# Kernel tuning notes

Measured on AMD Instinct MI355X. Metric: run time of the kernel, lower is better.

Reference implementation:

```python
import jax, jax.numpy as jnp
import numpy as np

N_NODES = 100000
N_EDGES = 1600000
IN_CH = 128
OUT_CH = 64
HEADS = 2
EDGE_DIM = 32


def _fake_quant(w):
    # 8-bit signed symmetric fake quantization (brevitas-style) with STE
    scale = jnp.max(jnp.abs(w)) / 127.0 + 1e-12
    q = jnp.clip(jnp.round(w / scale), -128.0, 127.0) * scale
    return w + jax.lax.stop_gradient(q - w)


def setup_inputs() -> dict:
    key = jax.random.key(0)
    ks = jax.random.split(key, 9)
    x = jax.random.normal(ks[0], (N_NODES, IN_CH), dtype=jnp.float32)
    edge_index = jax.random.randint(ks[1], (2, N_EDGES), 0, N_NODES, dtype=jnp.int64)
    edge_attr = jax.random.normal(ks[2], (N_EDGES, EDGE_DIM), dtype=jnp.float32)
    w_lin = jax.random.normal(ks[3], (HEADS * OUT_CH, IN_CH), dtype=jnp.float32) * (1.0 / np.sqrt(IN_CH))
    w_edge = jax.random.normal(ks[4], (HEADS * OUT_CH, EDGE_DIM), dtype=jnp.float32) * (1.0 / np.sqrt(EDGE_DIM))
    att_src = jax.random.normal(ks[5], (1, HEADS, OUT_CH), dtype=jnp.float32) * 0.1
    att_dst = jax.random.normal(ks[6], (1, HEADS, OUT_CH), dtype=jnp.float32) * 0.1
    att_edge = jax.random.normal(ks[7], (1, HEADS, OUT_CH), dtype=jnp.float32) * 0.1
    bias = jnp.zeros((OUT_CH,), dtype=jnp.float32)
    return {"x": x, "edge_index": edge_index, "edge_attr": edge_attr,
            "w_lin": w_lin, "w_edge": w_edge, "att_src": att_src,
            "att_dst": att_dst, "att_edge": att_edge, "bias": bias}


def reference(x, edge_index, edge_attr, w_lin, w_edge, att_src, att_dst, att_edge, bias):
    N = x.shape[0]
    src, dst = edge_index[0], edge_index[1]
    # quantized linear projection (int8 fake-quant weights)
    xp = (x @ _fake_quant(w_lin).T).reshape(N, HEADS, OUT_CH)  # [N,H,C]
    # per-node attention logits
    a_src = jnp.sum(xp * att_src, axis=-1)  # [N,H]
    a_dst = jnp.sum(xp * att_dst, axis=-1)  # [N,H]
    # edge feature projection + edge attention logits
    ep = (edge_attr @ w_edge.T).reshape(-1, HEADS, OUT_CH)      # [E,H,C]
    a_edge = jnp.sum(ep * att_edge, axis=-1)                    # [E,H]
    alpha = a_src[src] + a_dst[dst] + a_edge                    # [E,H]
    alpha = jax.nn.leaky_relu(alpha, negative_slope=0.2)
    # segment softmax over edges grouped by destination node
    amax = jax.ops.segment_max(alpha, dst, num_segments=N)      # [N,H]
    ex = jnp.exp(alpha - amax[dst])
    denom = jax.ops.segment_sum(ex, dst, num_segments=N)        # [N,H]
    coef = ex / (denom[dst] + 1e-16)                            # [E,H]
    # gather source messages, weight, scatter-add to destinations
    msg = xp[src] * coef[:, :, None]                            # [E,H,C]
    out = jax.ops.segment_sum(msg, dst, num_segments=N)         # [N,H,C]
    out = jnp.mean(out, axis=1) + bias                          # concat=False -> head mean
    # QuantIdentity on output (8-bit activation fake-quant)
    return _fake_quant(out)
```

## Files before the change

kernel.cpp:

```cpp
#include <hip/hip_runtime.h>
#include <math.h>

#define N_NODES 100000
#define N_EDGES 1600000
#define IN_CH 128
#define OUT_CH 64
#define HC 128
#define EDGE_DIM 32

__global__ __launch_bounds__(256) void k_prep(const float* __restrict__ w_lin,
                                              const float* __restrict__ w_edge,
                                              const float* __restrict__ att_edge,
                                              float* __restrict__ qw,
                                              float* __restrict__ ve) {
    __shared__ float red[256];
    __shared__ float sscale;
    int t = threadIdx.x;
    float m = 0.f;
    for (int i = t; i < HC * IN_CH; i += 256) m = fmaxf(m, fabsf(w_lin[i]));
    red[t] = m;
    __syncthreads();
    for (int off = 128; off > 0; off >>= 1) {
        if (t < off) red[t] = fmaxf(red[t], red[t + off]);
        __syncthreads();
    }
    if (t == 0) sscale = red[0] / 127.0f + 1e-12f;
    __syncthreads();
    float scale = sscale;
    for (int i = t; i < HC * IN_CH; i += 256) {
        float q = rintf(w_lin[i] / scale);
        q = fminf(127.f, fmaxf(-128.f, q));
        qw[i] = q * scale;
    }
    if (t < 64) {
        int h = t >> 5, k = t & 31;
        float s = 0.f;
        for (int c = 0; c < OUT_CH; ++c)
            s += att_edge[h * OUT_CH + c] * w_edge[(h * OUT_CH + c) * EDGE_DIM + k];
        ve[h * EDGE_DIM + k] = s;
    }
}

__global__ __launch_bounds__(256) void k_proj(const float* __restrict__ x,
                                              const float* __restrict__ qw,
                                              float* __restrict__ xp) {
    __shared__ float xs[128 * 128];
    const int nb = blockIdx.x * 128;
    for (int i = threadIdx.x; i < 4096; i += 256) {
        int w = i << 2;
        int row = w >> 7;
        int col = w & 127;
        int gn = nb + row;
        float4 v = make_float4(0.f, 0.f, 0.f, 0.f);
        if (gn < N_NODES) v = *(const float4*)(x + (size_t)gn * IN_CH + col);
        int scol = col ^ (((row >> 3) & 3) << 2);
        *(float4*)(&xs[row * 128 + scol]) = v;
    }
    __syncthreads();
    const int cg = threadIdx.x & 15;
    const int ng = threadIdx.x >> 4;
    const int c0 = cg << 3;
    const int n0 = ng << 3;
    float acc[8][8];
#pragma unroll
    for (int i = 0; i < 8; i++)
#pragma unroll
        for (int j = 0; j < 8; j++) acc[i][j] = 0.f;

    const int swz = ((ng & 3) << 2);
    for (int k = 0; k < 128; k += 4) {
        float4 xv[8], wv[8];
#pragma unroll
        for (int i = 0; i < 8; i++)
            xv[i] = *(const float4*)(&xs[(n0 + i) * 128 + (k ^ swz)]);
#pragma unroll
        for (int j = 0; j < 8; j++)
            wv[j] = *(const float4*)(qw + (c0 + j) * IN_CH + k);
#pragma unroll
        for (int i = 0; i < 8; i++)
#pragma unroll
            for (int j = 0; j < 8; j++)
                acc[i][j] += xv[i].x * wv[j].x + xv[i].y * wv[j].y +
                             xv[i].z * wv[j].z + xv[i].w * wv[j].w;
    }
#pragma unroll
    for (int i = 0; i < 8; i++) {
        int gn = nb + n0 + i;
        if (gn < N_NODES) {
            float4 o0 = make_float4(acc[i][0], acc[i][1], acc[i][2], acc[i][3]);
            float4 o1 = make_float4(acc[i][4], acc[i][5], acc[i][6], acc[i][7]);
            *(float4*)(xp + (size_t)gn * HC + c0) = o0;
            *(float4*)(xp + (size_t)gn * HC + c0 + 4) = o1;
        }
    }
}

__global__ __launch_bounds__(256) void k_attn_node(const float* __restrict__ xp,
                                                   const float* __restrict__ att_src,
                                                   const float* __restrict__ att_dst,
                                                   float* __restrict__ a_src,
                                                   float* __restrict__ a_dst) {
    int n = blockIdx.x * 4 + (threadIdx.x >> 6);
    int lane = threadIdx.x & 63;
    if (n >= N_NODES) return;
    float x0 = xp[(size_t)n * HC + lane];
    float x1 = xp[(size_t)n * HC + 64 + lane];
    float s0 = x0 * att_src[lane];
    float s1 = x1 * att_src[64 + lane];
    float d0 = x0 * att_dst[lane];
    float d1 = x1 * att_dst[64 + lane];
    for (int off = 32; off > 0; off >>= 1) {
        s0 += __shfl_xor(s0, off, 64);
        s1 += __shfl_xor(s1, off, 64);
        d0 += __shfl_xor(d0, off, 64);
        d1 += __shfl_xor(d1, off, 64);
    }
    if (lane == 0) {
        ((float2*)a_src)[n] = make_float2(s0, s1);
        ((float2*)a_dst)[n] = make_float2(d0, d1);
    }
}

__global__ __launch_bounds__(256) void k_edge(const int* __restrict__ ei,
                                              const float* __restrict__ ea,
                                              const float* __restrict__ ve,
                                              const float* __restrict__ a_src,
                                              const float* __restrict__ a_dst,
                                              float* __restrict__ alpha,
                                              int* __restrict__ counts) {
    __shared__ float lds[256 * 33];
    __shared__ float vel[64];
    int t = threadIdx.x;
    int base = blockIdx.x * 256;
    if (t < 64) vel[t] = ve[t];
    for (int i = t; i < 256 * EDGE_DIM; i += 256)
        lds[(i >> 5) * 33 + (i & 31)] = ea[(size_t)base * EDGE_DIM + i];
    __syncthreads();
    int e = base + t;
    int src = ei[e];
    int dst = ei[N_EDGES + e];
    float ae0 = 0.f, ae1 = 0.f;
    const float* row = &lds[t * 33];
#pragma unroll
    for (int k = 0; k < 32; k++) {
        ae0 += row[k] * vel[k];
        ae1 += row[k] * vel[32 + k];
    }
    float2 as = ((const float2*)a_src)[src];
    float2 ad = ((const float2*)a_dst)[dst];
    float al0 = as.x + ad.x + ae0;
    float al1 = as.y + ad.y + ae1;
    al0 = al0 >= 0.f ? al0 : 0.2f * al0;
    al1 = al1 >= 0.f ? al1 : 0.2f * al1;
    ((float2*)alpha)[e] = make_float2(al0, al1);
    atomicAdd(&counts[dst], 1);
}

__global__ __launch_bounds__(256) void k_bsum(const int* __restrict__ counts, int* __restrict__ bsums) {
    __shared__ int s[256];
    int i = blockIdx.x * 256 + threadIdx.x;
    int v = (i < N_NODES) ? counts[i] : 0;
    s[threadIdx.x] = v;
    __syncthreads();
    for (int off = 128; off > 0; off >>= 1) {
        if (threadIdx.x < off) s[threadIdx.x] += s[threadIdx.x + off];
        __syncthreads();
    }
    if (threadIdx.x == 0) bsums[blockIdx.x] = s[0];
}

__global__ __launch_bounds__(512) void k_bscan(const int* __restrict__ bsums, int* __restrict__ boff, int nb) {
    __shared__ int s[512];
    int t = threadIdx.x;
    int v = (t < nb) ? bsums[t] : 0;
    s[t] = v;
    __syncthreads();
    for (int off = 1; off < 512; off <<= 1) {
        int add = (t >= off) ? s[t - off] : 0;
        __syncthreads();
        s[t] += add;
        __syncthreads();
    }
    if (t < nb) boff[t] = s[t] - v;
}

__global__ __launch_bounds__(256) void k_offsets(const int* __restrict__ counts,
                                                 const int* __restrict__ boff,
                                                 int* __restrict__ offsets) {
    __shared__ int s[256];
    int t = threadIdx.x;
    int i = blockIdx.x * 256 + t;
    int v = (i < N_NODES) ? counts[i] : 0;
    s[t] = v;
    __syncthreads();
    for (int off = 1; off < 256; off <<= 1) {
        int add = (t >= off) ? s[t - off] : 0;
        __syncthreads();
        s[t] += add;
        __syncthreads();
    }
    if (i < N_NODES) offsets[i] = boff[blockIdx.x] + s[t] - v;
    if (i == 0) offsets[N_NODES] = N_EDGES;
}

__global__ __launch_bounds__(256) void k_scatter(const int* __restrict__ ei,
                                                 const float* __restrict__ alpha,
                                                 int* __restrict__ cursors,
                                                 int* __restrict__ src_sorted,
                                                 float* __restrict__ alpha_sorted) {
    int e = blockIdx.x * 256 + threadIdx.x;
    int src = ei[e];
    int dst = ei[N_EDGES + e];
    float2 a = ((const float2*)alpha)[e];
    int pos = atomicAdd(&cursors[dst], 1);
    src_sorted[pos] = src;
    ((float2*)alpha_sorted)[pos] = a;
}

__global__ __launch_bounds__(256) void k_aggregate(const int* __restrict__ offsets,
                                                   const int* __restrict__ src_sorted,
                                                   const float* __restrict__ alpha_sorted,
                                                   const float* __restrict__ xp,
                                                   const float* __restrict__ bias,
                                                   float* __restrict__ out) {
    int n = blockIdx.x * 4 + (threadIdx.x >> 6);
    if (n >= N_NODES) return;
    int lane = threadIdx.x & 63;
    int start = offsets[n], end = offsets[n + 1];
    float m0 = -INFINITY, m1 = -INFINITY;
    for (int j = start + lane; j < end; j += 64) {
        float2 a = ((const float2*)alpha_sorted)[j];
        m0 = fmaxf(m0, a.x);
        m1 = fmaxf(m1, a.y);
    }
    for (int off = 32; off > 0; off >>= 1) {
        m0 = fmaxf(m0, __shfl_xor(m0, off, 64));
        m1 = fmaxf(m1, __shfl_xor(m1, off, 64));
    }
    float accA = 0.f, accB = 0.f, d0 = 0.f, d1 = 0.f;
    int j = start;
    int s_next = 0;
    float2 a_next = make_float2(0.f, 0.f);
    if (j < end) {
        s_next = src_sorted[j];
        a_next = ((const float2*)alpha_sorted)[j];
    }
    for (; j < end; ++j) {
        int sc = s_next;
        float2 ac = a_next;
        if (j + 1 < end) {
            s_next = src_sorted[j + 1];
            a_next = ((const float2*)alpha_sorted)[j + 1];
        }
        float ex0 = expf(ac.x - m0);
        float ex1 = expf(ac.y - m1);
        d0 += ex0;
        d1 += ex1;
        const float* r = xp + (size_t)sc * HC;
        accA += ex0 * r[lane];
        accB += ex1 * r[64 + lane];
    }
    float o = 0.5f * (accA / (d0 + 1e-16f) + accB / (d1 + 1e-16f)) + bias[lane];
    out[(size_t)n * OUT_CH + lane] = o;
}

__global__ __launch_bounds__(256) void k_absmax(const float* __restrict__ v, unsigned int* __restrict__ amax) {
    float m = 0.f;
    int stride = gridDim.x * 256;
    for (int i = blockIdx.x * 256 + threadIdx.x; i < N_NODES * OUT_CH / 4; i += stride) {
        float4 x = ((const float4*)v)[i];
        m = fmaxf(m, fmaxf(fmaxf(fabsf(x.x), fabsf(x.y)), fmaxf(fabsf(x.z), fabsf(x.w))));
    }
    for (int off = 32; off > 0; off >>= 1) m = fmaxf(m, __shfl_xor(m, off, 64));
    if ((threadIdx.x & 63) == 0) atomicMax(amax, __float_as_uint(m));
}

__global__ __launch_bounds__(256) void k_quant_out(float* __restrict__ v, const unsigned int* __restrict__ amax) {
    float scale = __uint_as_float(*amax) / 127.0f + 1e-12f;
    int i = blockIdx.x * 256 + threadIdx.x;
    float4 x = ((const float4*)v)[i];
    float qx = fminf(127.f, fmaxf(-128.f, rintf(x.x / scale)));
    float qy = fminf(127.f, fmaxf(-128.f, rintf(x.y / scale)));
    float qz = fminf(127.f, fmaxf(-128.f, rintf(x.z / scale)));
    float qw_ = fminf(127.f, fmaxf(-128.f, rintf(x.w / scale)));
    ((float4*)v)[i] = make_float4(qx * scale, qy * scale, qz * scale, qw_ * scale);
}

extern "C" void kernel_launch(void* const* d_in, const int* in_sizes, int n_in,
                              void* d_out, int out_size, void* d_ws, size_t ws_size,
                              hipStream_t stream) {
    const float* x        = (const float*)d_in[0];
    const int*   ei       = (const int*)d_in[1];
    const float* ea       = (const float*)d_in[2];
    const float* w_lin    = (const float*)d_in[3];
    const float* w_edge   = (const float*)d_in[4];
    const float* att_src  = (const float*)d_in[5];
    const float* att_dst  = (const float*)d_in[6];
    const float* att_edge = (const float*)d_in[7];
    const float* bias     = (const float*)d_in[8];
    float* out = (float*)d_out;

    char* ws = (char*)d_ws;
    size_t off = 0;
    auto alloc = [&](size_t b) {
        void* p = ws + off;
        off = (off + b + 255) & ~(size_t)255;
        return p;
    };
    float* qw           = (float*)alloc((size_t)HC * IN_CH * 4);
    float* ve           = (float*)alloc(64 * 4);
    float* xp           = (float*)alloc((size_t)N_NODES * HC * 4);
    float* a_src        = (float*)alloc((size_t)N_NODES * 2 * 4);
    float* a_dst        = (float*)alloc((size_t)N_NODES * 2 * 4);
    float* alpha        = (float*)alloc((size_t)N_EDGES * 2 * 4);
    int*   counts       = (int*)alloc((size_t)N_NODES * 4);
    int*   offsets      = (int*)alloc((size_t)(N_NODES + 1) * 4);
    int*   cursors      = (int*)alloc((size_t)N_NODES * 4);
    int*   bsums        = (int*)alloc(512 * 4);
    int*   boff         = (int*)alloc(512 * 4);
    int*   src_sorted   = (int*)alloc((size_t)N_EDGES * 4);
    float* alpha_sorted = (float*)alloc((size_t)N_EDGES * 2 * 4);
    unsigned int* amax  = (unsigned int*)alloc(256);

    hipMemsetAsync(counts, 0, (size_t)N_NODES * 4, stream);
    hipMemsetAsync(amax, 0, 4, stream);

    k_prep<<<1, 256, 0, stream>>>(w_lin, w_edge, att_edge, qw, ve);
    k_proj<<<(N_NODES + 127) / 128, 256, 0, stream>>>(x, qw, xp);
    k_attn_node<<<(N_NODES + 3) / 4, 256, 0, stream>>>(xp, att_src, att_dst, a_src, a_dst);
    k_edge<<<N_EDGES / 256, 256, 0, stream>>>(ei, ea, ve, a_src, a_dst, alpha, counts);
    int nb = (N_NODES + 255) / 256;
    k_bsum<<<nb, 256, 0, stream>>>(counts, bsums);
    k_bscan<<<1, 512, 0, stream>>>(bsums, boff, nb);
    k_offsets<<<nb, 256, 0, stream>>>(counts, boff, offsets);
    hipMemcpyAsync(cursors, offsets, (size_t)N_NODES * 4, hipMemcpyDeviceToDevice, stream);
    k_scatter<<<N_EDGES / 256, 256, 0, stream>>>(ei, alpha, cursors, src_sorted, alpha_sorted);
    k_aggregate<<<(N_NODES + 3) / 4, 256, 0, stream>>>(offsets, src_sorted, alpha_sorted, xp, bias, out);
    k_absmax<<<1024, 256, 0, stream>>>(out, amax);
    k_quant_out<<<(N_NODES * OUT_CH / 4) / 256, 256, 0, stream>>>(out, amax);
}
```

Baseline: 880.8 us.

## Use bf16 MFMA split-precision projection, fuse node logits, merge alpha into scatter

The projection GEMM moves from fp32 FMA to bf16 MFMA. The int8-valued weights are stored exactly in bf16 and x is split into high and low bf16 parts to keep near-fp32 accuracy, with the scale applied afterwards. The node attention logits are computed in the GEMM epilogue, which removes a separate pass over xp. Edge alpha computation is moved into the scatter kernel, so the intermediate alpha array is no longer written and reread, and a light count kernel does the degree histogram. The aggregate kernel also switches to fast __expf, and the split-bf16 path adds a small rounding error compared with pure fp32.

```diff
diff --git a/kernel.cpp b/kernel.cpp
--- a/kernel.cpp
+++ b/kernel.cpp
@@ -8,10 +8,14 @@
 #define HC 128
 #define EDGE_DIM 32
 
+typedef __bf16 bf16x8 __attribute__((ext_vector_type(8)));
+typedef float f32x4 __attribute__((ext_vector_type(4)));
+
 __global__ __launch_bounds__(256) void k_prep(const float* __restrict__ w_lin,
                                               const float* __restrict__ w_edge,
                                               const float* __restrict__ att_edge,
-                                              float* __restrict__ qw,
+                                              __bf16* __restrict__ qwb,
+                                              float* __restrict__ qscale,
                                               float* __restrict__ ve) {
     __shared__ float red[256];
     __shared__ float sscale;
@@ -24,13 +28,13 @@
         if (t < off) red[t] = fmaxf(red[t], red[t + off]);
         __syncthreads();
     }
-    if (t == 0) sscale = red[0] / 127.0f + 1e-12f;
+    if (t == 0) { sscale = red[0] / 127.0f + 1e-12f; qscale[0] = sscale; }
     __syncthreads();
     float scale = sscale;
     for (int i = t; i < HC * IN_CH; i += 256) {
         float q = rintf(w_lin[i] / scale);
         q = fminf(127.f, fmaxf(-128.f, q));
-        qw[i] = q * scale;
+        qwb[i] = (__bf16)q;
     }
     if (t < 64) {
         int h = t >> 5, k = t & 31;
@@ -42,118 +46,124 @@
 }
 
 __global__ __launch_bounds__(256) void k_proj(const float* __restrict__ x,
-                                              const float* __restrict__ qw,
-                                              float* __restrict__ xp) {
-    __shared__ float xs[128 * 128];
-    const int nb = blockIdx.x * 128;
-    for (int i = threadIdx.x; i < 4096; i += 256) {
-        int w = i << 2;
-        int row = w >> 7;
-        int col = w & 127;
-        int gn = nb + row;
-        float4 v = make_float4(0.f, 0.f, 0.f, 0.f);
-        if (gn < N_NODES) v = *(const float4*)(x + (size_t)gn * IN_CH + col);
-        int scol = col ^ (((row >> 3) & 3) << 2);
-        *(float4*)(&xs[row * 128 + scol]) = v;
-    }
-    __syncthreads();
-    const int cg = threadIdx.x & 15;
-    const int ng = threadIdx.x >> 4;
-    const int c0 = cg << 3;
-    const int n0 = ng << 3;
-    float acc[8][8];
-#pragma unroll
-    for (int i = 0; i < 8; i++)
-#pragma unroll
-        for (int j = 0; j < 8; j++) acc[i][j] = 0.f;
-
-    const int swz = ((ng & 3) << 2);
-    for (int k = 0; k < 128; k += 4) {
-        float4 xv[8], wv[8];
-#pragma unroll
-        for (int i = 0; i < 8; i++)
-            xv[i] = *(const float4*)(&xs[(n0 + i) * 128 + (k ^ swz)]);
-#pragma unroll
-        for (int j = 0; j < 8; j++)
-            wv[j] = *(const float4*)(qw + (c0 + j) * IN_CH + k);
-#pragma unroll
-        for (int i = 0; i < 8; i++)
-#pragma unroll
-            for (int j = 0; j < 8; j++)
-                acc[i][j] += xv[i].x * wv[j].x + xv[i].y * wv[j].y +
-                             xv[i].z * wv[j].z + xv[i].w * wv[j].w;
-    }
-#pragma unroll
-    for (int i = 0; i < 8; i++) {
-        int gn = nb + n0 + i;
-        if (gn < N_NODES) {
-            float4 o0 = make_float4(acc[i][0], acc[i][1], acc[i][2], acc[i][3]);
-            float4 o1 = make_float4(acc[i][4], acc[i][5], acc[i][6], acc[i][7]);
-            *(float4*)(xp + (size_t)gn * HC + c0) = o0;
-            *(float4*)(xp + (size_t)gn * HC + c0 + 4) = o1;
-        }
-    }
-}
-
-__global__ __launch_bounds__(256) void k_attn_node(const float* __restrict__ xp,
-                                                   const float* __restrict__ att_src,
-                                                   const float* __restrict__ att_dst,
-                                                   float* __restrict__ a_src,
-                                                   float* __restrict__ a_dst) {
-    int n = blockIdx.x * 4 + (threadIdx.x >> 6);
-    int lane = threadIdx.x & 63;
-    if (n >= N_NODES) return;
-    float x0 = xp[(size_t)n * HC + lane];
-    float x1 = xp[(size_t)n * HC + 64 + lane];
-    float s0 = x0 * att_src[lane];
-    float s1 = x1 * att_src[64 + lane];
-    float d0 = x0 * att_dst[lane];
-    float d1 = x1 * att_dst[64 + lane];
-    for (int off = 32; off > 0; off >>= 1) {
-        s0 += __shfl_xor(s0, off, 64);
-        s1 += __shfl_xor(s1, off, 64);
-        d0 += __shfl_xor(d0, off, 64);
-        d1 += __shfl_xor(d1, off, 64);
-    }
-    if (lane == 0) {
-        ((float2*)a_src)[n] = make_float2(s0, s1);
-        ((float2*)a_dst)[n] = make_float2(d0, d1);
-    }
-}
-
-__global__ __launch_bounds__(256) void k_edge(const int* __restrict__ ei,
-                                              const float* __restrict__ ea,
-                                              const float* __restrict__ ve,
-                                              const float* __restrict__ a_src,
-                                              const float* __restrict__ a_dst,
-                                              float* __restrict__ alpha,
-                                              int* __restrict__ counts) {
-    __shared__ float lds[256 * 33];
-    __shared__ float vel[64];
-    int t = threadIdx.x;
-    int base = blockIdx.x * 256;
-    if (t < 64) vel[t] = ve[t];
-    for (int i = t; i < 256 * EDGE_DIM; i += 256)
-        lds[(i >> 5) * 33 + (i & 31)] = ea[(size_t)base * EDGE_DIM + i];
-    __syncthreads();
-    int e = base + t;
-    int src = ei[e];
-    int dst = ei[N_EDGES + e];
-    float ae0 = 0.f, ae1 = 0.f;
-    const float* row = &lds[t * 33];
-#pragma unroll
-    for (int k = 0; k < 32; k++) {
-        ae0 += row[k] * vel[k];
-        ae1 += row[k] * vel[32 + k];
-    }
-    float2 as = ((const float2*)a_src)[src];
-    float2 ad = ((const float2*)a_dst)[dst];
-    float al0 = as.x + ad.x + ae0;
-    float al1 = as.y + ad.y + ae1;
-    al0 = al0 >= 0.f ? al0 : 0.2f * al0;
-    al1 = al1 >= 0.f ? al1 : 0.2f * al1;
-    ((float2*)alpha)[e] = make_float2(al0, al1);
-    atomicAdd(&counts[dst], 1);
+                                              const __bf16* __restrict__ qwb,
+                                              const float* __restrict__ qscale,
+                                              const float* __restrict__ att_src,
+                                              const float* __restrict__ att_dst,
+                                              float* __restrict__ xp,
+                                              float* __restrict__ a_src,
+                                              float* __restrict__ a_dst) {
+    const int wave = threadIdx.x >> 6;
+    const int lane = threadIdx.x & 63;
+    const int cl = lane & 15;
+    const int kg = lane >> 4;
+    const int nb = blockIdx.x * 128 + wave * 32;
+
+    f32x4 acc[2][8];
+#pragma unroll
+    for (int mt = 0; mt < 2; ++mt)
+#pragma unroll
+        for (int nt = 0; nt < 8; ++nt)
+            acc[mt][nt] = (f32x4){0.f, 0.f, 0.f, 0.f};
+
+    const int kb0 = kg * 8;
+#pragma unroll
+    for (int kc = 0; kc < 4; ++kc) {
+        const int kb = kc * 32 + kb0;
+        bf16x8 ah[2], al[2];
+#pragma unroll
+        for (int mt = 0; mt < 2; ++mt) {
+            int row = nb + mt * 16 + cl;
+            float v[8];
+            if (row < N_NODES) {
+                f32x4 v0 = *(const f32x4*)(x + (size_t)row * IN_CH + kb);
+                f32x4 v1 = *(const f32x4*)(x + (size_t)row * IN_CH + kb + 4);
+                v[0] = v0.x; v[1] = v0.y; v[2] = v0.z; v[3] = v0.w;
+                v[4] = v1.x; v[5] = v1.y; v[6] = v1.z; v[7] = v1.w;
+            } else {
+#pragma unroll
+                for (int i = 0; i < 8; ++i) v[i] = 0.f;
+            }
+#pragma unroll
+            for (int i = 0; i < 8; ++i) {
+                __bf16 h = (__bf16)v[i];
+                ah[mt][i] = h;
+                al[mt][i] = (__bf16)(v[i] - (float)h);
+            }
+        }
+#pragma unroll
+        for (int nt = 0; nt < 8; ++nt) {
+            bf16x8 bw = *(const bf16x8*)(qwb + (size_t)(nt * 16 + cl) * IN_CH + kb);
+            acc[0][nt] = __builtin_amdgcn_mfma_f32_16x16x32_bf16(ah[0], bw, acc[0][nt], 0, 0, 0);
+            acc[0][nt] = __builtin_amdgcn_mfma_f32_16x16x32_bf16(al[0], bw, acc[0][nt], 0, 0, 0);
+            acc[1][nt] = __builtin_amdgcn_mfma_f32_16x16x32_bf16(ah[1], bw, acc[1][nt], 0, 0, 0);
+            acc[1][nt] = __builtin_amdgcn_mfma_f32_16x16x32_bf16(al[1], bw, acc[1][nt], 0, 0, 0);
+        }
+    }
+
+    const float scale = qscale[0];
+#pragma unroll
+    for (int mt = 0; mt < 2; ++mt)
+#pragma unroll
+        for (int nt = 0; nt < 8; ++nt)
+#pragma unroll
+            for (int r = 0; r < 4; ++r) acc[mt][nt][r] *= scale;
+
+#pragma unroll
+    for (int mt = 0; mt < 2; ++mt) {
+#pragma unroll
+        for (int r = 0; r < 4; ++r) {
+            int n = nb + mt * 16 + kg * 4 + r;
+            if (n < N_NODES) {
+#pragma unroll
+                for (int nt = 0; nt < 8; ++nt)
+                    xp[(size_t)n * HC + nt * 16 + cl] = acc[mt][nt][r];
+            }
+        }
+    }
+
+#pragma unroll
+    for (int mt = 0; mt < 2; ++mt) {
+        float s0[4] = {0.f, 0.f, 0.f, 0.f}, s1[4] = {0.f, 0.f, 0.f, 0.f};
+        float d0[4] = {0.f, 0.f, 0.f, 0.f}, d1[4] = {0.f, 0.f, 0.f, 0.f};
+#pragma unroll
+        for (int nt = 0; nt < 8; ++nt) {
+            int col = nt * 16 + cl;
+            float as_ = att_src[col];
+            float ad_ = att_dst[col];
+#pragma unroll
+            for (int r = 0; r < 4; ++r) {
+                float v = acc[mt][nt][r];
+                if (nt < 4) { s0[r] += v * as_; d0[r] += v * ad_; }
+                else        { s1[r] += v * as_; d1[r] += v * ad_; }
+            }
+        }
+#pragma unroll
+        for (int off = 1; off < 16; off <<= 1) {
+#pragma unroll
+            for (int r = 0; r < 4; ++r) {
+                s0[r] += __shfl_xor(s0[r], off, 64);
+                s1[r] += __shfl_xor(s1[r], off, 64);
+                d0[r] += __shfl_xor(d0[r], off, 64);
+                d1[r] += __shfl_xor(d1[r], off, 64);
+            }
+        }
+        if (cl == 0) {
+#pragma unroll
+            for (int r = 0; r < 4; ++r) {
+                int n = nb + mt * 16 + kg * 4 + r;
+                if (n < N_NODES) {
+                    ((float2*)a_src)[n] = make_float2(s0[r], s1[r]);
+                    ((float2*)a_dst)[n] = make_float2(d0[r], d1[r]);
+                }
+            }
+        }
+    }
+}
+
+__global__ __launch_bounds__(256) void k_count(const int* __restrict__ ei, int* __restrict__ counts) {
+    int e = blockIdx.x * 256 + threadIdx.x;
+    atomicAdd(&counts[ei[N_EDGES + e]], 1);
 }
 
 __global__ __launch_bounds__(256) void k_bsum(const int* __restrict__ counts, int* __restrict__ bsums) {
@@ -203,18 +213,41 @@
     if (i == 0) offsets[N_NODES] = N_EDGES;
 }
 
-__global__ __launch_bounds__(256) void k_scatter(const int* __restrict__ ei,
-                                                 const float* __restrict__ alpha,
-                                                 int* __restrict__ cursors,
-                                                 int* __restrict__ src_sorted,
-                                                 float* __restrict__ alpha_sorted) {
-    int e = blockIdx.x * 256 + threadIdx.x;
+__global__ __launch_bounds__(256) void k_scatter_alpha(const int* __restrict__ ei,
+                                                       const float* __restrict__ ea,
+                                                       const float* __restrict__ ve,
+                                                       const float* __restrict__ a_src,
+                                                       const float* __restrict__ a_dst,
+                                                       int* __restrict__ cursors,
+                                                       int* __restrict__ src_sorted,
+                                                       float* __restrict__ alpha_sorted) {
+    __shared__ float lds[256 * 33];
+    __shared__ float vel[64];
+    int t = threadIdx.x;
+    int base = blockIdx.x * 256;
+    if (t < 64) vel[t] = ve[t];
+    for (int i = t; i < 256 * EDGE_DIM; i += 256)
+        lds[(i >> 5) * 33 + (i & 31)] = ea[(size_t)base * EDGE_DIM + i];
+    __syncthreads();
+    int e = base + t;
     int src = ei[e];
     int dst = ei[N_EDGES + e];
-    float2 a = ((const float2*)alpha)[e];
+    float ae0 = 0.f, ae1 = 0.f;
+    const float* row = &lds[t * 33];
+#pragma unroll
+    for (int k = 0; k < 32; k++) {
+        ae0 += row[k] * vel[k];
+        ae1 += row[k] * vel[32 + k];
+    }
+    float2 as = ((const float2*)a_src)[src];
+    float2 ad = ((const float2*)a_dst)[dst];
+    float al0 = as.x + ad.x + ae0;
+    float al1 = as.y + ad.y + ae1;
+    al0 = al0 >= 0.f ? al0 : 0.2f * al0;
+    al1 = al1 >= 0.f ? al1 : 0.2f * al1;
     int pos = atomicAdd(&cursors[dst], 1);
     src_sorted[pos] = src;
-    ((float2*)alpha_sorted)[pos] = a;
+    ((float2*)alpha_sorted)[pos] = make_float2(al0, al1);
 }
 
 __global__ __launch_bounds__(256) void k_aggregate(const int* __restrict__ offsets,
@@ -252,8 +285,8 @@
             s_next = src_sorted[j + 1];
             a_next = ((const float2*)alpha_sorted)[j + 1];
         }
-        float ex0 = expf(ac.x - m0);
-        float ex1 = expf(ac.y - m1);
+        float ex0 = __expf(ac.x - m0);
+        float ex1 = __expf(ac.y - m1);
         d0 += ex0;
         d1 += ex1;
         const float* r = xp + (size_t)sc * HC;
@@ -307,12 +340,12 @@
         off = (off + b + 255) & ~(size_t)255;
         return p;
     };
-    float* qw           = (float*)alloc((size_t)HC * IN_CH * 4);
+    __bf16* qwb         = (__bf16*)alloc((size_t)HC * IN_CH * 2);
+    float* qscale       = (float*)alloc(256);
     float* ve           = (float*)alloc(64 * 4);
     float* xp           = (float*)alloc((size_t)N_NODES * HC * 4);
     float* a_src        = (float*)alloc((size_t)N_NODES * 2 * 4);
     float* a_dst        = (float*)alloc((size_t)N_NODES * 2 * 4);
-    float* alpha        = (float*)alloc((size_t)N_EDGES * 2 * 4);
     int*   counts       = (int*)alloc((size_t)N_NODES * 4);
     int*   offsets      = (int*)alloc((size_t)(N_NODES + 1) * 4);
     int*   cursors      = (int*)alloc((size_t)N_NODES * 4);
@@ -325,16 +358,15 @@
     hipMemsetAsync(counts, 0, (size_t)N_NODES * 4, stream);
     hipMemsetAsync(amax, 0, 4, stream);
 
-    k_prep<<<1, 256, 0, stream>>>(w_lin, w_edge, att_edge, qw, ve);
-    k_proj<<<(N_NODES + 127) / 128, 256, 0, stream>>>(x, qw, xp);
-    k_attn_node<<<(N_NODES + 3) / 4, 256, 0, stream>>>(xp, att_src, att_dst, a_src, a_dst);
-    k_edge<<<N_EDGES / 256, 256, 0, stream>>>(ei, ea, ve, a_src, a_dst, alpha, counts);
+    k_prep<<<1, 256, 0, stream>>>(w_lin, w_edge, att_edge, qwb, qscale, ve);
+    k_proj<<<(N_NODES + 127) / 128, 256, 0, stream>>>(x, qwb, qscale, att_src, att_dst, xp, a_src, a_dst);
+    k_count<<<N_EDGES / 256, 256, 0, stream>>>(ei, counts);
     int nb = (N_NODES + 255) / 256;
     k_bsum<<<nb, 256, 0, stream>>>(counts, bsums);
     k_bscan<<<1, 512, 0, stream>>>(bsums, boff, nb);
     k_offsets<<<nb, 256, 0, stream>>>(counts, boff, offsets);
     hipMemcpyAsync(cursors, offsets, (size_t)N_NODES * 4, hipMemcpyDeviceToDevice, stream);
-    k_scatter<<<N_EDGES / 256, 256, 0, stream>>>(ei, alpha, cursors, src_sorted, alpha_sorted);
+    k_scatter_alpha<<<N_EDGES / 256, 256, 0, stream>>>(ei, ea, ve, a_src, a_dst, cursors, src_sorted, alpha_sorted);
     k_aggregate<<<(N_NODES + 3) / 4, 256, 0, stream>>>(offsets, src_sorted, alpha_sorted, xp, bias, out);
     k_absmax<<<1024, 256, 0, stream>>>(out, amax);
     k_quant_out<<<(N_NODES * OUT_CH / 4) / 256, 256, 0, stream>>>(out, amax);
```

After: 730.8 us. -17.0%, faster.
